# Performance work log

Measured on AMD Instinct MI355X. Metric: run time of the kernel, lower is better.

The kernel has to match this reference:

```python
import jax, jax.numpy as jnp
import numpy as np

B, T, L, HE, HT, OUT = 512, 256, 256, 256, 512, 88

def _lin_init(key, fan_in, shape):
    bound = 1.0 / np.sqrt(fan_in)
    return jax.random.uniform(key, shape, minval=-bound, maxval=bound, dtype=jnp.float32)

def setup_inputs():
    key = jax.random.key(0)
    ks = jax.random.split(key, 19)
    p = {}
    p["z_hat"]  = jax.random.normal(ks[0], (B, T, L), dtype=jnp.float32)
    p["noise"]  = jax.random.normal(ks[1], (T, B, L), dtype=jnp.float32)  # randn_like per step
    p["z_init"] = jax.random.normal(ks[2], (B, L), dtype=jnp.float32)
    # emission MLP: L -> HE -> HE -> OUT
    p["We1"] = _lin_init(ks[3], L,  (L, HE));  p["be1"] = _lin_init(ks[4], L,  (HE,))
    p["We2"] = _lin_init(ks[5], HE, (HE, HE)); p["be2"] = _lin_init(ks[6], HE, (HE,))
    p["We3"] = _lin_init(ks[7], HE, (HE, OUT)); p["be3"] = _lin_init(ks[8], HE, (OUT,))
    # gate G: L -> HT -> L (sigmoid)
    p["Wg1"] = _lin_init(ks[9],  L,  (L, HT)); p["bg1"] = _lin_init(ks[10], L,  (HT,))
    p["Wg2"] = _lin_init(ks[11], HT, (HT, L)); p["bg2"] = _lin_init(ks[12], HT, (L,))
    # proposed mean H: L -> HT -> L
    p["Wh1"] = _lin_init(ks[13], L,  (L, HT)); p["bh1"] = _lin_init(ks[14], L,  (HT,))
    p["Wh2"] = _lin_init(ks[15], HT, (HT, L)); p["bh2"] = _lin_init(ks[16], HT, (L,))
    # mu_gated_linear: eye init weights, zero bias (square Linear per module init)
    p["Wmu"] = jnp.eye(L, dtype=jnp.float32)
    p["bmu"] = jnp.zeros((L,), dtype=jnp.float32)
    # sigma_gated_linear: ReLU -> Linear(L,L) -> Softplus
    p["Ws"] = _lin_init(ks[17], L, (L, L)); p["bs"] = _lin_init(ks[18], L, (L,))
    return p

def reference(z_hat, noise, z_init, We1, be1, We2, be2, We3, be3,
              Wg1, bg1, Wg2, bg2, Wh1, bh1, Wh2, bh2, Wmu, bmu, Ws, bs):
    # emission over all timesteps at once: [B,T,L] -> [B,T,OUT]
    h = jax.nn.relu(z_hat @ We1 + be1)
    h = jax.nn.relu(h @ We2 + be2)
    x_hat = jax.nn.sigmoid(h @ We3 + be3)

    # sequential transition with lax.scan; carry is z_prev [B,L]
    def step(z_prev, eps):
        g = jax.nn.sigmoid(jax.nn.relu(z_prev @ Wg1 + bg1) @ Wg2 + bg2)       # gate
        hh = jax.nn.relu(z_prev @ Wh1 + bh1) @ Wh2 + bh2                      # H(z_prev), computed once
        mu = hh * g + (z_prev @ Wmu + bmu) * (1.0 - g)                        # gated mean
        sigma = jax.nn.softplus(jax.nn.relu(hh) @ Ws + bs)                    # gated variance
        z_t = mu + jnp.sqrt(sigma) * eps                                      # reparam sample
        return z_t, (mu, sigma)

    _, (mus, sigmas) = jax.lax.scan(step, z_init, noise)  # stacked [T,B,L]
    mus = jnp.transpose(mus, (1, 0, 2))       # [B,T,L]
    sigmas = jnp.transpose(sigmas, (1, 0, 2)) # [B,T,L]
    return (x_hat, mus, sigmas)
```

## Files before the change

kernel.cpp:

```cpp
#include <hip/hip_runtime.h>
#include <cstddef>

#define B_ 512
#define T_ 256
#define L_ 256
#define HE_ 256
#define HT_ 512
#define OUT_ 88

__device__ __forceinline__ float sigmoidf_(float x) { return 1.f / (1.f + expf(-x)); }
__device__ __forceinline__ float softplusf_(float x) { return fmaxf(x, 0.f) + log1pf(expf(-fabsf(x))); }

#define EROWS 32

__device__ __forceinline__ void mlp_layer256(
    const float (*__restrict__ src)[256], float (*__restrict__ dst)[256],
    const float* __restrict__ W, const float* __restrict__ bias,
    int cx, int ry, bool do_relu)
{
  float acc[8][4] = {};
  for (int k = 0; k < 256; k += 4) {
    float sv[8][4];
    #pragma unroll
    for (int r = 0; r < 8; ++r) {
      float4 tv = *(const float4*)&src[ry * 8 + r][k];
      sv[r][0] = tv.x; sv[r][1] = tv.y; sv[r][2] = tv.z; sv[r][3] = tv.w;
    }
    #pragma unroll
    for (int kk = 0; kk < 4; ++kk) {
      float4 w = *(const float4*)&W[(size_t)(k + kk) * 256 + cx * 4];
      float wa[4] = {w.x, w.y, w.z, w.w};
      #pragma unroll
      for (int r = 0; r < 8; ++r) {
        #pragma unroll
        for (int j = 0; j < 4; ++j) acc[r][j] += sv[r][kk] * wa[j];
      }
    }
  }
  float4 bv = *(const float4*)&bias[cx * 4];
  float ba[4] = {bv.x, bv.y, bv.z, bv.w};
  #pragma unroll
  for (int r = 0; r < 8; ++r) {
    float v[4];
    #pragma unroll
    for (int j = 0; j < 4; ++j) {
      v[j] = acc[r][j] + ba[j];
      if (do_relu) v[j] = fmaxf(v[j], 0.f);
    }
    *(float4*)&dst[ry * 8 + r][cx * 4] = make_float4(v[0], v[1], v[2], v[3]);
  }
}

__global__ __launch_bounds__(256) void emission_kernel(
    const float* __restrict__ zhat,
    const float* __restrict__ We1, const float* __restrict__ be1,
    const float* __restrict__ We2, const float* __restrict__ be2,
    const float* __restrict__ We3, const float* __restrict__ be3,
    float* __restrict__ xhat)
{
  __shared__ __align__(16) float buf0[EROWS][256];
  __shared__ __align__(16) float buf1[EROWS][256];
  const int tid = threadIdx.x;
  const size_t row0 = (size_t)blockIdx.x * EROWS;

  {
    const float* src = zhat + row0 * 256;
    float* flat = &buf0[0][0];
    #pragma unroll
    for (int it = 0; it < 8; ++it) {
      int i = tid * 4 + it * 1024;
      *(float4*)&flat[i] = *(const float4*)&src[i];
    }
  }
  __syncthreads();

  const int cx = tid & 63;
  const int ry = tid >> 6;

  mlp_layer256(buf0, buf1, We1, be1, cx, ry, true);
  __syncthreads();
  mlp_layer256(buf1, buf0, We2, be2, cx, ry, true);
  __syncthreads();

  {
    const int lane = tid & 63;
    const bool has2 = (lane + 64) < OUT_;
    float acc1[8] = {}, acc2[8] = {};
    for (int k = 0; k < 256; k += 4) {
      float sv[8][4];
      #pragma unroll
      for (int r = 0; r < 8; ++r) {
        float4 tv = *(const float4*)&buf0[ry * 8 + r][k];
        sv[r][0] = tv.x; sv[r][1] = tv.y; sv[r][2] = tv.z; sv[r][3] = tv.w;
      }
      #pragma unroll
      for (int kk = 0; kk < 4; ++kk) {
        const size_t kw = (size_t)(k + kk) * OUT_;
        const float w1 = We3[kw + lane];
        const float w2 = has2 ? We3[kw + lane + 64] : 0.f;
        #pragma unroll
        for (int r = 0; r < 8; ++r) {
          acc1[r] += sv[r][kk] * w1;
          acc2[r] += sv[r][kk] * w2;
        }
      }
    }
    const float b1 = be3[lane];
    const float b2 = has2 ? be3[lane + 64] : 0.f;
    #pragma unroll
    for (int r = 0; r < 8; ++r) {
      const size_t orow = (row0 + ry * 8 + r) * OUT_;
      xhat[orow + lane] = sigmoidf_(acc1[r] + b1);
      if (has2) xhat[orow + lane + 64] = sigmoidf_(acc2[r] + b2);
    }
  }
}

#define MROWS 4

__global__ __launch_bounds__(512) void transition_kernel(
    const float* __restrict__ noise, const float* __restrict__ z_init,
    const float* __restrict__ Wg1, const float* __restrict__ bg1,
    const float* __restrict__ Wg2, const float* __restrict__ bg2,
    const float* __restrict__ Wh1, const float* __restrict__ bh1,
    const float* __restrict__ Wh2, const float* __restrict__ bh2,
    const float* __restrict__ Wmu, const float* __restrict__ bmu,
    const float* __restrict__ Ws, const float* __restrict__ bs,
    float* __restrict__ mus, float* __restrict__ sigmas)
{
  __shared__ __align__(16) float zb[MROWS][L_];
  __shared__ __align__(16) float a1g[MROWS][HT_];
  __shared__ __align__(16) float a1h[MROWS][HT_];
  __shared__ __align__(16) float gb[MROWS][L_];
  __shared__ __align__(16) float hb[MROWS][L_];
  __shared__ __align__(16) float scratch[8192];

  const int tid = threadIdx.x;
  const int b0 = blockIdx.x * MROWS;

  const int cgA = tid & 127;
  const int pA_ = (tid >> 7) & 1;
  const int kqA = tid >> 8;
  const float* __restrict__ W1 = pA_ ? Wh1 : Wg1;

  const int cgB = tid & 63;
  const int pB_ = (tid >> 6) & 1;
  const int kqB = tid >> 7;
  const float* __restrict__ W2 = pB_ ? Wh2 : Wg2;
  const float* __restrict__ W3 = pB_ ? Wmu : Ws;

  for (int i = tid; i < MROWS * L_; i += 512)
    zb[i >> 8][i & 255] = z_init[(size_t)(b0 + (i >> 8)) * L_ + (i & 255)];
  __syncthreads();

  for (int t = 0; t < T_; ++t) {
    {
      float acc[MROWS][4] = {};
      const int k0 = kqA * 128;
      #pragma unroll 2
      for (int k = k0; k < k0 + 128; k += 4) {
        float zv[MROWS][4];
        #pragma unroll
        for (int r = 0; r < MROWS; ++r) {
          float4 tv = *(const float4*)&zb[r][k];
          zv[r][0] = tv.x; zv[r][1] = tv.y; zv[r][2] = tv.z; zv[r][3] = tv.w;
        }
        #pragma unroll
        for (int kk = 0; kk < 4; ++kk) {
          float4 w = *(const float4*)&W1[(size_t)(k + kk) * HT_ + cgA * 4];
          float wa[4] = {w.x, w.y, w.z, w.w};
          #pragma unroll
          for (int r = 0; r < MROWS; ++r)
            #pragma unroll
            for (int j = 0; j < 4; ++j) acc[r][j] += zv[r][kk] * wa[j];
        }
      }
      #pragma unroll
      for (int r = 0; r < MROWS; ++r)
        *(float4*)&scratch[(size_t)(((kqA * 2 + pA_) * 4 + r) * 512) + cgA * 4] =
            make_float4(acc[r][0], acc[r][1], acc[r][2], acc[r][3]);
    }
    __syncthreads();

    #pragma unroll
    for (int i = 0; i < 8; ++i) {
      int idx = tid + i * 512;
      int c = idx & 511; int rp = idx >> 9; int r = rp & 3; int p = rp >> 2;
      float v = scratch[((0 * 2 + p) * 4 + r) * 512 + c]
              + scratch[((1 * 2 + p) * 4 + r) * 512 + c]
              + (p ? bh1[c] : bg1[c]);
      v = fmaxf(v, 0.f);
      if (p) a1h[r][c] = v; else a1g[r][c] = v;
    }
    __syncthreads();

    {
      const float (*__restrict__ srcB)[HT_] = pB_ ? a1h : a1g;
      float acc[MROWS][4] = {};
      const int k0 = kqB * 128;
      #pragma unroll 2
      for (int k = k0; k < k0 + 128; k += 4) {
        float av[MROWS][4];
        #pragma unroll
        for (int r = 0; r < MROWS; ++r) {
          float4 tv = *(const float4*)&srcB[r][k];
          av[r][0] = tv.x; av[r][1] = tv.y; av[r][2] = tv.z; av[r][3] = tv.w;
        }
        #pragma unroll
        for (int kk = 0; kk < 4; ++kk) {
          float4 w = *(const float4*)&W2[(size_t)(k + kk) * L_ + cgB * 4];
          float wa[4] = {w.x, w.y, w.z, w.w};
          #pragma unroll
          for (int r = 0; r < MROWS; ++r)
            #pragma unroll
            for (int j = 0; j < 4; ++j) acc[r][j] += av[r][kk] * wa[j];
        }
      }
      #pragma unroll
      for (int r = 0; r < MROWS; ++r)
        *(float4*)&scratch[(size_t)(((kqB * 2 + pB_) * 4 + r) * 256) + cgB * 4] =
            make_float4(acc[r][0], acc[r][1], acc[r][2], acc[r][3]);
    }
    __syncthreads();

    #pragma unroll
    for (int i = 0; i < 4; ++i) {
      int idx = tid + i * 512;
      int c = idx & 255; int rp = idx >> 8; int r = rp & 3; int p = rp >> 2;
      float s = scratch[((0 * 2 + p) * 4 + r) * 256 + c]
              + scratch[((1 * 2 + p) * 4 + r) * 256 + c]
              + scratch[((2 * 2 + p) * 4 + r) * 256 + c]
              + scratch[((3 * 2 + p) * 4 + r) * 256 + c];
      if (p) hb[r][c] = s + bh2[c];
      else   gb[r][c] = sigmoidf_(s + bg2[c]);
    }
    __syncthreads();

    {
      float acc[MROWS][4] = {};
      const int k0 = kqB * 64;
      #pragma unroll 2
      for (int k = k0; k < k0 + 64; k += 4) {
        float sv[MROWS][4];
        #pragma unroll
        for (int r = 0; r < MROWS; ++r) {
          if (pB_) {
            float4 tv = *(const float4*)&zb[r][k];
            sv[r][0] = tv.x; sv[r][1] = tv.y; sv[r][2] = tv.z; sv[r][3] = tv.w;
          } else {
            float4 tv = *(const float4*)&hb[r][k];
            sv[r][0] = fmaxf(tv.x, 0.f); sv[r][1] = fmaxf(tv.y, 0.f);
            sv[r][2] = fmaxf(tv.z, 0.f); sv[r][3] = fmaxf(tv.w, 0.f);
          }
        }
        #pragma unroll
        for (int kk = 0; kk < 4; ++kk) {
          float4 w = *(const float4*)&W3[(size_t)(k + kk) * L_ + cgB * 4];
          float wa[4] = {w.x, w.y, w.z, w.w};
          #pragma unroll
          for (int r = 0; r < MROWS; ++r)
            #pragma unroll
            for (int j = 0; j < 4; ++j) acc[r][j] += sv[r][kk] * wa[j];
        }
      }
      #pragma unroll
      for (int r = 0; r < MROWS; ++r)
        *(float4*)&scratch[(size_t)(((kqB * 2 + pB_) * 4 + r) * 256) + cgB * 4] =
            make_float4(acc[r][0], acc[r][1], acc[r][2], acc[r][3]);
    }
    __syncthreads();

    #pragma unroll
    for (int i = 0; i < 2; ++i) {
      int idx = tid + i * 512;
      int c = idx & 255; int r = idx >> 8;
      float sp = scratch[((0 * 2 + 0) * 4 + r) * 256 + c]
               + scratch[((1 * 2 + 0) * 4 + r) * 256 + c]
               + scratch[((2 * 2 + 0) * 4 + r) * 256 + c]
               + scratch[((3 * 2 + 0) * 4 + r) * 256 + c] + bs[c];
      float ml = scratch[((0 * 2 + 1) * 4 + r) * 256 + c]
               + scratch[((1 * 2 + 1) * 4 + r) * 256 + c]
               + scratch[((2 * 2 + 1) * 4 + r) * 256 + c]
               + scratch[((3 * 2 + 1) * 4 + r) * 256 + c] + bmu[c];
      float g = gb[r][c], h = hb[r][c];
      float sigma = softplusf_(sp);
      float mu = h * g + ml * (1.f - g);
      float eps = noise[((size_t)t * B_ + (b0 + r)) * L_ + c];
      float zn = mu + sqrtf(sigma) * eps;
      size_t o = ((size_t)(b0 + r) * T_ + t) * L_ + c;
      mus[o] = mu;
      sigmas[o] = sigma;
      zb[r][c] = zn;
    }
    __syncthreads();
  }
}

extern "C" void kernel_launch(void* const* d_in, const int* in_sizes, int n_in,
                              void* d_out, int out_size, void* d_ws, size_t ws_size,
                              hipStream_t stream)
{
  (void)in_sizes; (void)n_in; (void)d_ws; (void)ws_size; (void)out_size;
  const float* z_hat  = (const float*)d_in[0];
  const float* noise  = (const float*)d_in[1];
  const float* z_init = (const float*)d_in[2];
  const float* We1 = (const float*)d_in[3];  const float* be1 = (const float*)d_in[4];
  const float* We2 = (const float*)d_in[5];  const float* be2 = (const float*)d_in[6];
  const float* We3 = (const float*)d_in[7];  const float* be3 = (const float*)d_in[8];
  const float* Wg1 = (const float*)d_in[9];  const float* bg1 = (const float*)d_in[10];
  const float* Wg2 = (const float*)d_in[11]; const float* bg2 = (const float*)d_in[12];
  const float* Wh1 = (const float*)d_in[13]; const float* bh1 = (const float*)d_in[14];
  const float* Wh2 = (const float*)d_in[15]; const float* bh2 = (const float*)d_in[16];
  const float* Wmu = (const float*)d_in[17]; const float* bmu = (const float*)d_in[18];
  const float* Ws  = (const float*)d_in[19]; const float* bs  = (const float*)d_in[20];

  float* out    = (float*)d_out;
  float* xhat   = out;
  float* mus    = out + (size_t)B_ * T_ * OUT_;
  float* sigmas = mus + (size_t)B_ * T_ * L_;

  hipLaunchKernelGGL(transition_kernel, dim3(B_ / MROWS), dim3(512), 0, stream,
                     noise, z_init, Wg1, bg1, Wg2, bg2, Wh1, bh1, Wh2, bh2,
                     Wmu, bmu, Ws, bs, mus, sigmas);
  hipLaunchKernelGGL(emission_kernel, dim3((B_ * T_) / EROWS), dim3(256), 0, stream,
                     z_hat, We1, be1, We2, be2, We3, be3, xhat);
}
```

Baseline: 6.648 ms.

## Fuse transition and emission into one kernel with 1024-thread blocks

```diff
diff --git a/kernel.cpp b/kernel.cpp
--- a/kernel.cpp
+++ b/kernel.cpp
@@ -4,26 +4,28 @@
 #define B_ 512
 #define T_ 256
 #define L_ 256
-#define HE_ 256
 #define HT_ 512
 #define OUT_ 88
 
+#define MROWS 4
+#define NTB (B_ / MROWS)
+#define EROWS 32
+#define NEB ((B_ * T_) / EROWS)
+
 __device__ __forceinline__ float sigmoidf_(float x) { return 1.f / (1.f + expf(-x)); }
 __device__ __forceinline__ float softplusf_(float x) { return fmaxf(x, 0.f) + log1pf(expf(-fabsf(x))); }
 
-#define EROWS 32
-
-__device__ __forceinline__ void mlp_layer256(
+__device__ __forceinline__ void em_layer256(
     const float (*__restrict__ src)[256], float (*__restrict__ dst)[256],
     const float* __restrict__ W, const float* __restrict__ bias,
-    int cx, int ry, bool do_relu)
+    int cx, int ry)
 {
-  float acc[8][4] = {};
+  float acc[2][4] = {};
   for (int k = 0; k < 256; k += 4) {
-    float sv[8][4];
+    float sv[2][4];
     #pragma unroll
-    for (int r = 0; r < 8; ++r) {
-      float4 tv = *(const float4*)&src[ry * 8 + r][k];
+    for (int r = 0; r < 2; ++r) {
+      float4 tv = *(const float4*)&src[ry * 2 + r][k];
       sv[r][0] = tv.x; sv[r][1] = tv.y; sv[r][2] = tv.z; sv[r][3] = tv.w;
     }
     #pragma unroll
@@ -31,268 +33,256 @@
       float4 w = *(const float4*)&W[(size_t)(k + kk) * 256 + cx * 4];
       float wa[4] = {w.x, w.y, w.z, w.w};
       #pragma unroll
-      for (int r = 0; r < 8; ++r) {
+      for (int r = 0; r < 2; ++r)
         #pragma unroll
         for (int j = 0; j < 4; ++j) acc[r][j] += sv[r][kk] * wa[j];
-      }
     }
   }
   float4 bv = *(const float4*)&bias[cx * 4];
   float ba[4] = {bv.x, bv.y, bv.z, bv.w};
   #pragma unroll
-  for (int r = 0; r < 8; ++r) {
+  for (int r = 0; r < 2; ++r) {
     float v[4];
     #pragma unroll
-    for (int j = 0; j < 4; ++j) {
-      v[j] = acc[r][j] + ba[j];
-      if (do_relu) v[j] = fmaxf(v[j], 0.f);
-    }
-    *(float4*)&dst[ry * 8 + r][cx * 4] = make_float4(v[0], v[1], v[2], v[3]);
+    for (int j = 0; j < 4; ++j) v[j] = fmaxf(acc[r][j] + ba[j], 0.f);
+    *(float4*)&dst[ry * 2 + r][cx * 4] = make_float4(v[0], v[1], v[2], v[3]);
   }
 }
 
-__global__ __launch_bounds__(256) void emission_kernel(
+__global__ __launch_bounds__(1024, 4) void fused_kernel(
     const float* __restrict__ zhat,
+    const float* __restrict__ noise, const float* __restrict__ z_init,
     const float* __restrict__ We1, const float* __restrict__ be1,
     const float* __restrict__ We2, const float* __restrict__ be2,
     const float* __restrict__ We3, const float* __restrict__ be3,
-    float* __restrict__ xhat)
-{
-  __shared__ __align__(16) float buf0[EROWS][256];
-  __shared__ __align__(16) float buf1[EROWS][256];
-  const int tid = threadIdx.x;
-  const size_t row0 = (size_t)blockIdx.x * EROWS;
-
-  {
-    const float* src = zhat + row0 * 256;
-    float* flat = &buf0[0][0];
-    #pragma unroll
-    for (int it = 0; it < 8; ++it) {
-      int i = tid * 4 + it * 1024;
-      *(float4*)&flat[i] = *(const float4*)&src[i];
-    }
-  }
-  __syncthreads();
-
-  const int cx = tid & 63;
-  const int ry = tid >> 6;
-
-  mlp_layer256(buf0, buf1, We1, be1, cx, ry, true);
-  __syncthreads();
-  mlp_layer256(buf1, buf0, We2, be2, cx, ry, true);
-  __syncthreads();
-
-  {
-    const int lane = tid & 63;
-    const bool has2 = (lane + 64) < OUT_;
-    float acc1[8] = {}, acc2[8] = {};
-    for (int k = 0; k < 256; k += 4) {
-      float sv[8][4];
-      #pragma unroll
-      for (int r = 0; r < 8; ++r) {
-        float4 tv = *(const float4*)&buf0[ry * 8 + r][k];
-        sv[r][0] = tv.x; sv[r][1] = tv.y; sv[r][2] = tv.z; sv[r][3] = tv.w;
-      }
-      #pragma unroll
-      for (int kk = 0; kk < 4; ++kk) {
-        const size_t kw = (size_t)(k + kk) * OUT_;
-        const float w1 = We3[kw + lane];
-        const float w2 = has2 ? We3[kw + lane + 64] : 0.f;
-        #pragma unroll
-        for (int r = 0; r < 8; ++r) {
-          acc1[r] += sv[r][kk] * w1;
-          acc2[r] += sv[r][kk] * w2;
-        }
-      }
-    }
-    const float b1 = be3[lane];
-    const float b2 = has2 ? be3[lane + 64] : 0.f;
-    #pragma unroll
-    for (int r = 0; r < 8; ++r) {
-      const size_t orow = (row0 + ry * 8 + r) * OUT_;
-      xhat[orow + lane] = sigmoidf_(acc1[r] + b1);
-      if (has2) xhat[orow + lane + 64] = sigmoidf_(acc2[r] + b2);
-    }
-  }
-}
-
-#define MROWS 4
-
-__global__ __launch_bounds__(512) void transition_kernel(
-    const float* __restrict__ noise, const float* __restrict__ z_init,
     const float* __restrict__ Wg1, const float* __restrict__ bg1,
     const float* __restrict__ Wg2, const float* __restrict__ bg2,
     const float* __restrict__ Wh1, const float* __restrict__ bh1,
     const float* __restrict__ Wh2, const float* __restrict__ bh2,
     const float* __restrict__ Wmu, const float* __restrict__ bmu,
     const float* __restrict__ Ws, const float* __restrict__ bs,
-    float* __restrict__ mus, float* __restrict__ sigmas)
+    float* __restrict__ xhat, float* __restrict__ mus, float* __restrict__ sigmas)
 {
-  __shared__ __align__(16) float zb[MROWS][L_];
-  __shared__ __align__(16) float a1g[MROWS][HT_];
-  __shared__ __align__(16) float a1h[MROWS][HT_];
-  __shared__ __align__(16) float gb[MROWS][L_];
-  __shared__ __align__(16) float hb[MROWS][L_];
-  __shared__ __align__(16) float scratch[8192];
-
+  __shared__ __align__(16) char pool[94208];
   const int tid = threadIdx.x;
-  const int b0 = blockIdx.x * MROWS;
-
-  const int cgA = tid & 127;
-  const int pA_ = (tid >> 7) & 1;
-  const int kqA = tid >> 8;
-  const float* __restrict__ W1 = pA_ ? Wh1 : Wg1;
-
-  const int cgB = tid & 63;
-  const int pB_ = (tid >> 6) & 1;
-  const int kqB = tid >> 7;
-  const float* __restrict__ W2 = pB_ ? Wh2 : Wg2;
-  const float* __restrict__ W3 = pB_ ? Wmu : Ws;
-
-  for (int i = tid; i < MROWS * L_; i += 512)
-    zb[i >> 8][i & 255] = z_init[(size_t)(b0 + (i >> 8)) * L_ + (i & 255)];
-  __syncthreads();
-
-  for (int t = 0; t < T_; ++t) {
+
+  if (blockIdx.x < NTB) {
+    float (*zb)[L_]   = (float(*)[L_])(pool);
+    float (*a1g)[HT_] = (float(*)[HT_])(pool + 4096);
+    float (*a1h)[HT_] = (float(*)[HT_])(pool + 12288);
+    float (*gb)[L_]   = (float(*)[L_])(pool + 20480);
+    float (*hb)[L_]   = (float(*)[L_])(pool + 24576);
+    float* scratch    = (float*)(pool + 28672);
+
+    const int b0 = blockIdx.x * MROWS;
+
+    const int cgA = tid & 127;
+    const int pA_ = (tid >> 7) & 1;
+    const int kqA = tid >> 8;
+    const float* __restrict__ W1 = pA_ ? Wh1 : Wg1;
+    const int cgB = tid & 63;
+    const int pB_ = (tid >> 6) & 1;
+    const int kqB = tid >> 7;
+    const float* __restrict__ W2 = pB_ ? Wh2 : Wg2;
+    const float* __restrict__ W3 = pB_ ? Wmu : Ws;
+
+    zb[tid >> 8][tid & 255] = z_init[(size_t)(b0 + (tid >> 8)) * L_ + (tid & 255)];
+    __syncthreads();
+
+    for (int t = 0; t < T_; ++t) {
+      {
+        float acc[MROWS][4] = {};
+        const int k0 = kqA * 64;
+        #pragma unroll 2
+        for (int k = k0; k < k0 + 64; k += 4) {
+          float zv[MROWS][4];
+          #pragma unroll
+          for (int r = 0; r < MROWS; ++r) {
+            float4 tv = *(const float4*)&zb[r][k];
+            zv[r][0] = tv.x; zv[r][1] = tv.y; zv[r][2] = tv.z; zv[r][3] = tv.w;
+          }
+          #pragma unroll
+          for (int kk = 0; kk < 4; ++kk) {
+            float4 w = *(const float4*)&W1[(size_t)(k + kk) * HT_ + cgA * 4];
+            float wa[4] = {w.x, w.y, w.z, w.w};
+            #pragma unroll
+            for (int r = 0; r < MROWS; ++r)
+              #pragma unroll
+              for (int j = 0; j < 4; ++j) acc[r][j] += zv[r][kk] * wa[j];
+          }
+        }
+        #pragma unroll
+        for (int r = 0; r < MROWS; ++r)
+          *(float4*)&scratch[(((kqA * 2 + pA_) * 4 + r) * 512) + cgA * 4] =
+              make_float4(acc[r][0], acc[r][1], acc[r][2], acc[r][3]);
+      }
+      __syncthreads();
+
+      #pragma unroll
+      for (int i = 0; i < 4; ++i) {
+        int idx = tid + i * 1024;
+        int c = idx & 511; int rp = idx >> 9; int r = rp & 3; int p = rp >> 2;
+        float v = scratch[((0 * 2 + p) * 4 + r) * 512 + c]
+                + scratch[((1 * 2 + p) * 4 + r) * 512 + c]
+                + scratch[((2 * 2 + p) * 4 + r) * 512 + c]
+                + scratch[((3 * 2 + p) * 4 + r) * 512 + c]
+                + (p ? bh1[c] : bg1[c]);
+        v = fmaxf(v, 0.f);
+        if (p) a1h[r][c] = v; else a1g[r][c] = v;
+      }
+      __syncthreads();
+
+      {
+        const float (*__restrict__ srcB)[HT_] = pB_ ? a1h : a1g;
+        float acc[MROWS][4] = {};
+        const int k0 = kqB * 64;
+        #pragma unroll 2
+        for (int k = k0; k < k0 + 64; k += 4) {
+          float av[MROWS][4];
+          #pragma unroll
+          for (int r = 0; r < MROWS; ++r) {
+            float4 tv = *(const float4*)&srcB[r][k];
+            av[r][0] = tv.x; av[r][1] = tv.y; av[r][2] = tv.z; av[r][3] = tv.w;
+          }
+          #pragma unroll
+          for (int kk = 0; kk < 4; ++kk) {
+            float4 w = *(const float4*)&W2[(size_t)(k + kk) * L_ + cgB * 4];
+            float wa[4] = {w.x, w.y, w.z, w.w};
+            #pragma unroll
+            for (int r = 0; r < MROWS; ++r)
+              #pragma unroll
+              for (int j = 0; j < 4; ++j) acc[r][j] += av[r][kk] * wa[j];
+          }
+        }
+        #pragma unroll
+        for (int r = 0; r < MROWS; ++r)
+          *(float4*)&scratch[(((kqB * 2 + pB_) * 4 + r) * 256) + cgB * 4] =
+              make_float4(acc[r][0], acc[r][1], acc[r][2], acc[r][3]);
+      }
+      __syncthreads();
+
+      #pragma unroll
+      for (int i = 0; i < 2; ++i) {
+        int idx = tid + i * 1024;
+        int c = idx & 255; int rp = idx >> 8; int r = rp & 3; int p = rp >> 2;
+        float s = 0.f;
+        #pragma unroll
+        for (int kq = 0; kq < 8; ++kq)
+          s += scratch[((kq * 2 + p) * 4 + r) * 256 + c];
+        if (p) hb[r][c] = s + bh2[c];
+        else   gb[r][c] = sigmoidf_(s + bg2[c]);
+      }
+      __syncthreads();
+
+      {
+        float acc[MROWS][4] = {};
+        const int k0 = kqB * 32;
+        #pragma unroll 2
+        for (int k = k0; k < k0 + 32; k += 4) {
+          float sv[MROWS][4];
+          #pragma unroll
+          for (int r = 0; r < MROWS; ++r) {
+            if (pB_) {
+              float4 tv = *(const float4*)&zb[r][k];
+              sv[r][0] = tv.x; sv[r][1] = tv.y; sv[r][2] = tv.z; sv[r][3] = tv.w;
+            } else {
+              float4 tv = *(const float4*)&hb[r][k];
+              sv[r][0] = fmaxf(tv.x, 0.f); sv[r][1] = fmaxf(tv.y, 0.f);
+              sv[r][2] = fmaxf(tv.z, 0.f); sv[r][3] = fmaxf(tv.w, 0.f);
+            }
+          }
+          #pragma unroll
+          for (int kk = 0; kk < 4; ++kk) {
+            float4 w = *(const float4*)&W3[(size_t)(k + kk) * L_ + cgB * 4];
+            float wa[4] = {w.x, w.y, w.z, w.w};
+            #pragma unroll
+            for (int r = 0; r < MROWS; ++r)
+              #pragma unroll
+              for (int j = 0; j < 4; ++j) acc[r][j] += sv[r][kk] * wa[j];
+          }
+        }
+        #pragma unroll
+        for (int r = 0; r < MROWS; ++r)
+          *(float4*)&scratch[(((kqB * 2 + pB_) * 4 + r) * 256) + cgB * 4] =
+              make_float4(acc[r][0], acc[r][1], acc[r][2], acc[r][3]);
+      }
+      __syncthreads();
+
+      {
+        int c = tid & 255; int r = tid >> 8;
+        float sp = bs[c], ml = bmu[c];
+        #pragma unroll
+        for (int kq = 0; kq < 8; ++kq) {
+          sp += scratch[((kq * 2 + 0) * 4 + r) * 256 + c];
+          ml += scratch[((kq * 2 + 1) * 4 + r) * 256 + c];
+        }
+        float g = gb[r][c], h = hb[r][c];
+        float sigma = softplusf_(sp);
+        float mu = h * g + ml * (1.f - g);
+        float eps = noise[((size_t)t * B_ + (b0 + r)) * L_ + c];
+        size_t o = ((size_t)(b0 + r) * T_ + t) * L_ + c;
+        mus[o] = mu;
+        sigmas[o] = sigma;
+        zb[r][c] = mu + sqrtf(sigma) * eps;
+      }
+      __syncthreads();
+    }
+  } else {
+    float (*buf0)[256] = (float(*)[256])(pool);
+    float (*buf1)[256] = (float(*)[256])(pool + 32768);
+    const size_t row0 = (size_t)(blockIdx.x - NTB) * EROWS;
+
     {
-      float acc[MROWS][4] = {};
-      const int k0 = kqA * 128;
-      #pragma unroll 2
-      for (int k = k0; k < k0 + 128; k += 4) {
-        float zv[MROWS][4];
-        #pragma unroll
-        for (int r = 0; r < MROWS; ++r) {
-          float4 tv = *(const float4*)&zb[r][k];
-          zv[r][0] = tv.x; zv[r][1] = tv.y; zv[r][2] = tv.z; zv[r][3] = tv.w;
+      const float* src = zhat + row0 * 256;
+      float* flat = &buf0[0][0];
+      #pragma unroll
+      for (int it = 0; it < 2; ++it) {
+        int i = (tid + it * 1024) * 4;
+        *(float4*)&flat[i] = *(const float4*)&src[i];
+      }
+    }
+    __syncthreads();
+
+    const int cx = tid & 63;
+    const int ry = tid >> 6;
+
+    em_layer256(buf0, buf1, We1, be1, cx, ry);
+    __syncthreads();
+    em_layer256(buf1, buf0, We2, be2, cx, ry);
+    __syncthreads();
+
+    {
+      const int lane = tid & 63;
+      const bool has2 = (lane + 64) < OUT_;
+      float acc1[2] = {}, acc2[2] = {};
+      for (int k = 0; k < 256; k += 4) {
+        float sv[2][4];
+        #pragma unroll
+        for (int r = 0; r < 2; ++r) {
+          float4 tv = *(const float4*)&buf0[ry * 2 + r][k];
+          sv[r][0] = tv.x; sv[r][1] = tv.y; sv[r][2] = tv.z; sv[r][3] = tv.w;
         }
         #pragma unroll
         for (int kk = 0; kk < 4; ++kk) {
-          float4 w = *(const float4*)&W1[(size_t)(k + kk) * HT_ + cgA * 4];
-          float wa[4] = {w.x, w.y, w.z, w.w};
-          #pragma unroll
-          for (int r = 0; r < MROWS; ++r)
-            #pragma unroll
-            for (int j = 0; j < 4; ++j) acc[r][j] += zv[r][kk] * wa[j];
-        }
-      }
-      #pragma unroll
-      for (int r = 0; r < MROWS; ++r)
-        *(float4*)&scratch[(size_t)(((kqA * 2 + pA_) * 4 + r) * 512) + cgA * 4] =
-            make_float4(acc[r][0], acc[r][1], acc[r][2], acc[r][3]);
-    }
-    __syncthreads();
-
-    #pragma unroll
-    for (int i = 0; i < 8; ++i) {
-      int idx = tid + i * 512;
-      int c = idx & 511; int rp = idx >> 9; int r = rp & 3; int p = rp >> 2;
-      float v = scratch[((0 * 2 + p) * 4 + r) * 512 + c]
-              + scratch[((1 * 2 + p) * 4 + r) * 512 + c]
-              + (p ? bh1[c] : bg1[c]);
-      v = fmaxf(v, 0.f);
-      if (p) a1h[r][c] = v; else a1g[r][c] = v;
-    }
-    __syncthreads();
-
-    {
-      const float (*__restrict__ srcB)[HT_] = pB_ ? a1h : a1g;
-      float acc[MROWS][4] = {};
-      const int k0 = kqB * 128;
-      #pragma unroll 2
-      for (int k = k0; k < k0 + 128; k += 4) {
-        float av[MROWS][4];
-        #pragma unroll
-        for (int r = 0; r < MROWS; ++r) {
-          float4 tv = *(const float4*)&srcB[r][k];
-          av[r][0] = tv.x; av[r][1] = tv.y; av[r][2] = tv.z; av[r][3] = tv.w;
-        }
-        #pragma unroll
-        for (int kk = 0; kk < 4; ++kk) {
-          float4 w = *(const float4*)&W2[(size_t)(k + kk) * L_ + cgB * 4];
-          float wa[4] = {w.x, w.y, w.z, w.w};
-          #pragma unroll
-          for (int r = 0; r < MROWS; ++r)
-            #pragma unroll
-            for (int j = 0; j < 4; ++j) acc[r][j] += av[r][kk] * wa[j];
-        }
-      }
-      #pragma unroll
-      for (int r = 0; r < MROWS; ++r)
-        *(float4*)&scratch[(size_t)(((kqB * 2 + pB_) * 4 + r) * 256) + cgB * 4] =
-            make_float4(acc[r][0], acc[r][1], acc[r][2], acc[r][3]);
-    }
-    __syncthreads();
-
-    #pragma unroll
-    for (int i = 0; i < 4; ++i) {
-      int idx = tid + i * 512;
-      int c = idx & 255; int rp = idx >> 8; int r = rp & 3; int p = rp >> 2;
-      float s = scratch[((0 * 2 + p) * 4 + r) * 256 + c]
-              + scratch[((1 * 2 + p) * 4 + r) * 256 + c]
-              + scratch[((2 * 2 + p) * 4 + r) * 256 + c]
-              + scratch[((3 * 2 + p) * 4 + r) * 256 + c];
-      if (p) hb[r][c] = s + bh2[c];
-      else   gb[r][c] = sigmoidf_(s + bg2[c]);
-    }
-    __syncthreads();
-
-    {
-      float acc[MROWS][4] = {};
-      const int k0 = kqB * 64;
-      #pragma unroll 2
-      for (int k = k0; k < k0 + 64; k += 4) {
-        float sv[MROWS][4];
-        #pragma unroll
-        for (int r = 0; r < MROWS; ++r) {
-          if (pB_) {
-            float4 tv = *(const float4*)&zb[r][k];
-            sv[r][0] = tv.x; sv[r][1] = tv.y; sv[r][2] = tv.z; sv[r][3] = tv.w;
-          } else {
-            float4 tv = *(const float4*)&hb[r][k];
-            sv[r][0] = fmaxf(tv.x, 0.f); sv[r][1] = fmaxf(tv.y, 0.f);
-            sv[r][2] = fmaxf(tv.z, 0.f); sv[r][3] = fmaxf(tv.w, 0.f);
-          }
-        }
-        #pragma unroll
-        for (int kk = 0; kk < 4; ++kk) {
-          float4 w = *(const float4*)&W3[(size_t)(k + kk) * L_ + cgB * 4];
-          float wa[4] = {w.x, w.y, w.z, w.w};
-          #pragma unroll
-          for (int r = 0; r < MROWS; ++r)
-            #pragma unroll
-            for (int j = 0; j < 4; ++j) acc[r][j] += sv[r][kk] * wa[j];
-        }
-      }
-      #pragma unroll
-      for (int r = 0; r < MROWS; ++r)
-        *(float4*)&scratch[(size_t)(((kqB * 2 + pB_) * 4 + r) * 256) + cgB * 4] =
-            make_float4(acc[r][0], acc[r][1], acc[r][2], acc[r][3]);
-    }
-    __syncthreads();
-
-    #pragma unroll
-    for (int i = 0; i < 2; ++i) {
-      int idx = tid + i * 512;
-      int c = idx & 255; int r = idx >> 8;
-      float sp = scratch[((0 * 2 + 0) * 4 + r) * 256 + c]
-               + scratch[((1 * 2 + 0) * 4 + r) * 256 + c]
-               + scratch[((2 * 2 + 0) * 4 + r) * 256 + c]
-               + scratch[((3 * 2 + 0) * 4 + r) * 256 + c] + bs[c];
-      float ml = scratch[((0 * 2 + 1) * 4 + r) * 256 + c]
-               + scratch[((1 * 2 + 1) * 4 + r) * 256 + c]
-               + scratch[((2 * 2 + 1) * 4 + r) * 256 + c]
-               + scratch[((3 * 2 + 1) * 4 + r) * 256 + c] + bmu[c];
-      float g = gb[r][c], h = hb[r][c];
-      float sigma = softplusf_(sp);
-      float mu = h * g + ml * (1.f - g);
-      float eps = noise[((size_t)t * B_ + (b0 + r)) * L_ + c];
-      float zn = mu + sqrtf(sigma) * eps;
-      size_t o = ((size_t)(b0 + r) * T_ + t) * L_ + c;
-      mus[o] = mu;
-      sigmas[o] = sigma;
-      zb[r][c] = zn;
-    }
-    __syncthreads();
+          const size_t kw = (size_t)(k + kk) * OUT_;
+          const float w1 = We3[kw + lane];
+          const float w2 = has2 ? We3[kw + lane + 64] : 0.f;
+          #pragma unroll
+          for (int r = 0; r < 2; ++r) {
+            acc1[r] += sv[r][kk] * w1;
+            acc2[r] += sv[r][kk] * w2;
+          }
+        }
+      }
+      const float b1 = be3[lane];
+      const float b2 = has2 ? be3[lane + 64] : 0.f;
+      #pragma unroll
+      for (int r = 0; r < 2; ++r) {
+        const size_t orow = (row0 + ry * 2 + r) * OUT_;
+        xhat[orow + lane] = sigmoidf_(acc1[r] + b1);
+        if (has2) xhat[orow + lane + 64] = sigmoidf_(acc2[r] + b2);
+      }
+    }
   }
 }
 
@@ -319,9 +309,8 @@
   float* mus    = out + (size_t)B_ * T_ * OUT_;
   float* sigmas = mus + (size_t)B_ * T_ * L_;
 
-  hipLaunchKernelGGL(transition_kernel, dim3(B_ / MROWS), dim3(512), 0, stream,
-                     noise, z_init, Wg1, bg1, Wg2, bg2, Wh1, bh1, Wh2, bh2,
-                     Wmu, bmu, Ws, bs, mus, sigmas);
-  hipLaunchKernelGGL(emission_kernel, dim3((B_ * T_) / EROWS), dim3(256), 0, stream,
-                     z_hat, We1, be1, We2, be2, We3, be3, xhat);
+  hipLaunchKernelGGL(fused_kernel, dim3(NTB + NEB), dim3(1024), 0, stream,
+                     z_hat, noise, z_init, We1, be1, We2, be2, We3, be3,
+                     Wg1, bg1, Wg2, bg2, Wh1, bh1, Wh2, bh2,
+                     Wmu, bmu, Ws, bs, xhat, mus, sigmas);
 }
```

After: 6.347 ms. -4.5%, faster.
